# Kernel tuning notes

Hardware: AMD Instinct MI355X
Metric: run time of the kernel (lower is better)

## Reference

```python
import jax, jax.numpy as jnp
import numpy as np

HID = 128
H = 96
W = 96
WS = 6      # window_size
SS = 3      # shift_size
LN_EPS = 1e-5


def _layer_norm(x, g, b):
    m = x.mean(-1, keepdims=True)
    v = ((x - m) ** 2).mean(-1, keepdims=True)
    return (x - m) / jnp.sqrt(v + LN_EPS) * g + b


def _block(x, Wm, bm, g, bg):
    # Linear -> LayerNorm -> GELU (dropout is identity at inference)
    return jax.nn.gelu(_layer_norm(x @ Wm + bm, g, bg), approximate=False)


def _window_context(grid, Wt, bt, gt, bgt):
    # grid: [B, H, W, D]. Window partition + mean over the ws*ws tokens is
    # equivalent to a mean over each (ws, ws) tile; broadcasting back is a repeat.
    B, Hh, Ww, D = grid.shape
    nh, nw = Hh // WS, Ww // WS
    win_mean = grid.reshape(B, nh, WS, nw, WS, D).mean(axis=(2, 4))  # [B, nh, nw, D]
    tok = _block(win_mean, Wt, bt, gt, bgt)                          # token_proj
    return jnp.repeat(jnp.repeat(tok, WS, axis=1), WS, axis=2)       # [B, H, W, D]


def setup_inputs() -> dict:
    key = jax.random.key(0)
    ks = jax.random.split(key, 8)
    B = 32
    s = 1.0 / np.sqrt(HID)
    inp = {
        "h_pixel": jax.random.normal(ks[0], (B, H * W, HID), dtype=jnp.float32),
        "node_mask": jnp.ones((B, H * W), dtype=jnp.float32),
        # token_proj: Linear(D,D) + LayerNorm(D)
        "Wt": jax.random.normal(ks[1], (HID, HID), dtype=jnp.float32) * s,
        "bt": jnp.zeros((HID,), jnp.float32),
        "gt": jnp.ones((HID,), jnp.float32),
        "bgt": jnp.zeros((HID,), jnp.float32),
        # fuse: Linear(D,D) + LayerNorm(D)  (regular_shifted_sum -> fuse_in = D)
        "Wf": jax.random.normal(ks[2], (HID, HID), dtype=jnp.float32) * s,
        "bf": jnp.zeros((HID,), jnp.float32),
        "gf": jnp.ones((HID,), jnp.float32),
        "bgf": jnp.zeros((HID,), jnp.float32),
        # out_proj: Linear(D,D) + LayerNorm(D)
        "Wo": jax.random.normal(ks[3], (HID, HID), dtype=jnp.float32) * s,
        "bo": jnp.zeros((HID,), jnp.float32),
        "go": jnp.ones((HID,), jnp.float32),
        "bgo": jnp.zeros((HID,), jnp.float32),
    }
    return inp


def reference(h_pixel, node_mask, Wt, bt, gt, bgt, Wf, bf, gf, bgf, Wo, bo, go, bgo):
    B, N, D = h_pixel.shape
    grid = h_pixel.reshape(B, H, W, D)
    reg = _window_context(grid, Wt, bt, gt, bgt)
    shifted = jnp.roll(grid, (-SS, -SS), axis=(1, 2))
    sh = _window_context(shifted, Wt, bt, gt, bgt)
    sh = jnp.roll(sh, (SS, SS), axis=(1, 2))
    ctx = _block(reg + sh, Wf, bf, gf, bgf)     # fuse
    out = _block(ctx, Wo, bo, go, bgo)          # out_proj
    out = out.reshape(B, N, D) * node_mask[..., None]
    return out
```

## Files before the change

### kernel.cpp

```cpp
#include <hip/hip_runtime.h>
#include <hip/hip_bf16.h>


#define DEVFN static __device__ __forceinline__

typedef __attribute__((ext_vector_type(8))) short bf16x8;
typedef __attribute__((ext_vector_type(16))) float f32x16;

DEVFN float gelu_exact(float x) {
  return 0.5f * x * (1.0f + erff(x * 0.70710678118654752f));
}

DEVFN unsigned short f2bf(float f) {
  unsigned int u = __float_as_uint(f);
  u = (u + 0x7FFFu + ((u >> 16) & 1u)) >> 16;
  return (unsigned short)u;
}

DEVFN float bf2f(unsigned short u) {
  return __uint_as_float((unsigned int)u << 16);
}

DEVFN void add4(float4& a, const float4 v) {
  a.x += v.x; a.y += v.y; a.z += v.z; a.w += v.w;
}
DEVFN void fma4(float4& a, const float4 v, float m) {
  a.x = fmaf(v.x, m, a.x); a.y = fmaf(v.y, m, a.y);
  a.z = fmaf(v.z, m, a.z); a.w = fmaf(v.w, m, a.w);
}

__global__ __launch_bounds__(512) void k_tile3(const float* __restrict__ h,
                                               unsigned short* __restrict__ S3) {
  const int b  = blockIdx.x >> 5;
  const int ry = blockIdx.x & 31;
  const int w    = threadIdx.x >> 6;
  const int lane = threadIdx.x & 63;
  const int half = lane >> 5;
  const int ch4  = (lane & 31) << 2;
  const float mlo = half ? 0.f : 1.f;
  const float mhi = 1.f - mlo;

  float4 acc[4];
  #pragma unroll
  for (int t = 0; t < 4; ++t) acc[t] = make_float4(0.f, 0.f, 0.f, 0.f);

  #pragma unroll
  for (int yy = 0; yy < 3; ++yy) {
    const float* rp =
        h + ((size_t)(b * 9216 + (3 * ry + yy) * 96 + 12 * w + half) * 128 + ch4);
    #pragma unroll
    for (int j = 0; j < 6; ++j) {
      const float4 v = *reinterpret_cast<const float4*>(rp + j * 256);
      if (j == 0)      add4(acc[0], v);
      else if (j == 2) add4(acc[1], v);
      else if (j == 3) add4(acc[2], v);
      else if (j == 5) add4(acc[3], v);
      else if (j == 1) { fma4(acc[0], v, mlo); fma4(acc[1], v, mhi); }
      else             { fma4(acc[2], v, mlo); fma4(acc[3], v, mhi); }
    }
  }

  #pragma unroll
  for (int t = 0; t < 4; ++t) {
    float4 s = acc[t];
    s.x += __shfl_xor(s.x, 32, 64);
    s.y += __shfl_xor(s.y, 32, 64);
    s.z += __shfl_xor(s.z, 32, 64);
    s.w += __shfl_xor(s.w, 32, 64);
    if (half == 0) {
      short4 pk;
      pk.x = (short)f2bf(s.x); pk.y = (short)f2bf(s.y);
      pk.z = (short)f2bf(s.z); pk.w = (short)f2bf(s.w);
      *reinterpret_cast<short4*>(
          &S3[((size_t)(b * 32 + ry) * 32 + 4 * w + t) * 128 + ch4]) = pk;
    }
  }
}

DEVFN void stage_w_bf(unsigned short* __restrict__ wl,
                      const float* __restrict__ W, int tid) {
  #pragma unroll
  for (int p = 0; p < 4; ++p) {
    const int i = tid + p * 512;
    const int kp = i >> 5;
    const int n4 = (i & 31) * 4;
    const float4 r0 = *reinterpret_cast<const float4*>(W + (size_t)(2 * kp) * 128 + n4);
    const float4 r1 = *reinterpret_cast<const float4*>(W + (size_t)(2 * kp + 1) * 128 + n4);
    const float a0[4] = {r0.x, r0.y, r0.z, r0.w};
    const float a1[4] = {r1.x, r1.y, r1.z, r1.w};
    #pragma unroll
    for (int j = 0; j < 4; ++j) {
      const unsigned int pk =
          (unsigned int)f2bf(a0[j]) | ((unsigned int)f2bf(a1[j]) << 16);
      *reinterpret_cast<unsigned int*>(&wl[(n4 + j) * 136 + 2 * kp]) = pk;
    }
  }
}

DEVFN f32x16 mfma_tile(const unsigned short* __restrict__ xrow,
                       const unsigned short* __restrict__ wrow) {
  f32x16 acc;
  #pragma unroll
  for (int r = 0; r < 16; ++r) acc[r] = 0.f;
  #pragma unroll
  for (int kk = 0; kk < 8; ++kk) {
    const bf16x8 a = *reinterpret_cast<const bf16x8*>(xrow + kk * 16);
    const bf16x8 bb = *reinterpret_cast<const bf16x8*>(wrow + kk * 16);
    acc = __builtin_amdgcn_mfma_f32_32x32x16_bf16(a, bb, acc, 0, 0, 0);
  }
  return acc;
}

DEVFN void write_raw(float* __restrict__ raw, const f32x16 acc,
                     int tg, int cg, int lane) {
  const int n  = cg * 32 + (lane & 31);
  const int mb = tg * 32 + 4 * (lane >> 5);
  #pragma unroll
  for (int r = 0; r < 16; ++r) {
    const int mm = mb + (r & 3) + 8 * (r >> 2);
    raw[mm * 132 + n] = acc[r];
  }
}

__global__ __launch_bounds__(512) void k_tok(const unsigned short* __restrict__ S3,
    const float* __restrict__ Wt, const float* __restrict__ bt,
    const float* __restrict__ gt, const float* __restrict__ bgt,
    float* __restrict__ tok) {
  __shared__ __align__(16) unsigned short xs_bf[64 * 136];
  __shared__ __align__(16) unsigned short wl[128 * 136];
  float* raw = reinterpret_cast<float*>(wl);

  const int tid = threadIdx.x;
  const int t0 = blockIdx.x * 64;
  const int s  = t0 >> 13;
  const int b  = (t0 >> 8) & 31;
  const int wyx = t0 & 255;

  const unsigned short* Sb = S3 + (size_t)b * 131072;
  #pragma unroll
  for (int p = 0; p < 2; ++p) {
    const int i = tid + p * 512;
    const int tt = i >> 4, c8 = (i & 15) * 8;
    const int idx = wyx + tt;
    const int wy = idx >> 4, wx = idx & 15;
    int ry0, ry1, c0, c1;
    if (s == 0) { ry0 = 2 * wy;     ry1 = 2 * wy + 1;        c0 = 2 * wx;     c1 = 2 * wx + 1; }
    else        { ry0 = 2 * wy + 1; ry1 = (2 * wy + 2) & 31; c0 = 2 * wx + 1; c1 = (2 * wx + 2) & 31; }
    const bf16x8 v00 = *reinterpret_cast<const bf16x8*>(Sb + ((size_t)(ry0 * 32 + c0) * 128 + c8));
    const bf16x8 v01 = *reinterpret_cast<const bf16x8*>(Sb + ((size_t)(ry0 * 32 + c1) * 128 + c8));
    const bf16x8 v10 = *reinterpret_cast<const bf16x8*>(Sb + ((size_t)(ry1 * 32 + c0) * 128 + c8));
    const bf16x8 v11 = *reinterpret_cast<const bf16x8*>(Sb + ((size_t)(ry1 * 32 + c1) * 128 + c8));
    bf16x8 pk;
    #pragma unroll
    for (int j = 0; j < 8; ++j) {
      const float sum = bf2f((unsigned short)v00[j]) + bf2f((unsigned short)v01[j]) +
                        bf2f((unsigned short)v10[j]) + bf2f((unsigned short)v11[j]);
      pk[j] = (short)f2bf(sum * (1.f / 36.f));
    }
    *reinterpret_cast<bf16x8*>(&xs_bf[tt * 136 + c8]) = pk;
  }
  stage_w_bf(wl, Wt, tid);
  __syncthreads();

  const int lane = tid & 63;
  const int w = tid >> 6;
  const int tg = w >> 2, cg = w & 3;
  const unsigned short* xrow = &xs_bf[(tg * 32 + (lane & 31)) * 136 + 8 * (lane >> 5)];
  const unsigned short* wrow = &wl[(cg * 32 + (lane & 31)) * 136 + 8 * (lane >> 5)];

  const f32x16 acc = mfma_tile(xrow, wrow);
  __syncthreads();
  write_raw(raw, acc, tg, cg, lane);
  __syncthreads();

  {
    const int tt = tid >> 3, cb = tid & 7;
    float v[16];
    float s2 = 0.f, q = 0.f;
    #pragma unroll
    for (int i = 0; i < 4; ++i) {
      const int col = 4 * cb + 32 * i;
      const float4 rv = *reinterpret_cast<const float4*>(&raw[tt * 132 + col]);
      const float4 bv = *reinterpret_cast<const float4*>(bt + col);
      v[4 * i + 0] = rv.x + bv.x; v[4 * i + 1] = rv.y + bv.y;
      v[4 * i + 2] = rv.z + bv.z; v[4 * i + 3] = rv.w + bv.w;
    }
    #pragma unroll
    for (int e = 0; e < 16; ++e) { s2 += v[e]; q += v[e] * v[e]; }
    s2 += __shfl_xor(s2, 1, 8); q += __shfl_xor(q, 1, 8);
    s2 += __shfl_xor(s2, 2, 8); q += __shfl_xor(q, 2, 8);
    s2 += __shfl_xor(s2, 4, 8); q += __shfl_xor(q, 4, 8);
    const float mean = s2 * (1.f / 128.f);
    const float var  = q * (1.f / 128.f) - mean * mean;
    const float inv  = rsqrtf(var + 1e-5f);
    #pragma unroll
    for (int i = 0; i < 4; ++i) {
      const int col = 4 * cb + 32 * i;
      const float4 gv = *reinterpret_cast<const float4*>(gt + col);
      const float4 ev = *reinterpret_cast<const float4*>(bgt + col);
      float4 ov;
      ov.x = gelu_exact((v[4 * i + 0] - mean) * inv * gv.x + ev.x);
      ov.y = gelu_exact((v[4 * i + 1] - mean) * inv * gv.y + ev.y);
      ov.z = gelu_exact((v[4 * i + 2] - mean) * inv * gv.z + ev.z);
      ov.w = gelu_exact((v[4 * i + 3] - mean) * inv * gv.w + ev.w);
      *reinterpret_cast<float4*>(tok + (size_t)(t0 + tt) * 128 + col) = ov;
    }
  }
}

__global__ __launch_bounds__(512) void k_fuse_out(const float* __restrict__ tok,
    const float* __restrict__ Wf, const float* __restrict__ bfv,
    const float* __restrict__ gf, const float* __restrict__ bgf,
    const float* __restrict__ Wo, const float* __restrict__ bo,
    const float* __restrict__ go, const float* __restrict__ bgo,
    const float* __restrict__ mask, float* __restrict__ out) {
  __shared__ __align__(16) unsigned short xs_bf[64 * 136];
  __shared__ __align__(16) unsigned short wl[128 * 136];
  float* raw = reinterpret_cast<float*>(wl);

  const int tid = threadIdx.x;
  const int b = blockIdx.x >> 4;
  const int m = blockIdx.x & 15;
  const int lane = tid & 63;
  const int w = tid >> 6;
  const int tg = w >> 2, cg = w & 3;

  const float* tokR = tok + (size_t)b * 32768 + (size_t)m * 2048;
  const float* tokS = tok + 1048576 + (size_t)b * 32768;

  #pragma unroll
  for (int p = 0; p < 2; ++p) {
    const int i = tid + p * 512;
    const int t = i >> 4, c8 = (i & 15) * 8;
    const int gx = t & 31, gy = 2 * m + (t >> 5);
    const int wx  = gx >> 1;
    const int wxs = ((gx + 31) & 31) >> 1;
    const int wys = ((gy + 31) & 31) >> 1;
    const float* pr = tokR + (size_t)wx * 128 + c8;
    const float* ps = tokS + (size_t)(wys * 16 + wxs) * 128 + c8;
    bf16x8 pk;
    #pragma unroll
    for (int j = 0; j < 8; ++j)
      pk[j] = (short)f2bf(pr[j] + ps[j]);
    *reinterpret_cast<bf16x8*>(&xs_bf[t * 136 + c8]) = pk;
  }
  stage_w_bf(wl, Wf, tid);
  __syncthreads();

  const unsigned short* xrow = &xs_bf[(tg * 32 + (lane & 31)) * 136 + 8 * (lane >> 5)];
  const unsigned short* wrow = &wl[(cg * 32 + (lane & 31)) * 136 + 8 * (lane >> 5)];

  const f32x16 acc1 = mfma_tile(xrow, wrow);
  __syncthreads();
  write_raw(raw, acc1, tg, cg, lane);
  __syncthreads();

  {
    const int tt = tid >> 3, cb = tid & 7;
    float v[16];
    float s = 0.f, q = 0.f;
    #pragma unroll
    for (int i = 0; i < 4; ++i) {
      const int col = 4 * cb + 32 * i;
      const float4 rv = *reinterpret_cast<const float4*>(&raw[tt * 132 + col]);
      const float4 bv = *reinterpret_cast<const float4*>(bfv + col);
      v[4 * i + 0] = rv.x + bv.x; v[4 * i + 1] = rv.y + bv.y;
      v[4 * i + 2] = rv.z + bv.z; v[4 * i + 3] = rv.w + bv.w;
    }
    #pragma unroll
    for (int e = 0; e < 16; ++e) { s += v[e]; q += v[e] * v[e]; }
    s += __shfl_xor(s, 1, 8); q += __shfl_xor(q, 1, 8);
    s += __shfl_xor(s, 2, 8); q += __shfl_xor(q, 2, 8);
    s += __shfl_xor(s, 4, 8); q += __shfl_xor(q, 4, 8);
    const float mean = s * (1.f / 128.f);
    const float var  = q * (1.f / 128.f) - mean * mean;
    const float inv  = rsqrtf(var + 1e-5f);
    __syncthreads();
    #pragma unroll
    for (int i = 0; i < 4; ++i) {
      const int col = 4 * cb + 32 * i;
      const float4 gv = *reinterpret_cast<const float4*>(gf + col);
      const float4 ev = *reinterpret_cast<const float4*>(bgf + col);
      short4 pk;
      pk.x = (short)f2bf(gelu_exact((v[4 * i + 0] - mean) * inv * gv.x + ev.x));
      pk.y = (short)f2bf(gelu_exact((v[4 * i + 1] - mean) * inv * gv.y + ev.y));
      pk.z = (short)f2bf(gelu_exact((v[4 * i + 2] - mean) * inv * gv.z + ev.z));
      pk.w = (short)f2bf(gelu_exact((v[4 * i + 3] - mean) * inv * gv.w + ev.w));
      *reinterpret_cast<short4*>(&xs_bf[tt * 136 + col]) = pk;
    }
  }
  __syncthreads();
  stage_w_bf(wl, Wo, tid);
  __syncthreads();

  const f32x16 acc2 = mfma_tile(xrow, wrow);
  __syncthreads();
  write_raw(raw, acc2, tg, cg, lane);
  __syncthreads();

  {
    const int tt = tid >> 3, cb = tid & 7;
    float v[16];
    float s = 0.f, q = 0.f;
    #pragma unroll
    for (int i = 0; i < 4; ++i) {
      const int col = 4 * cb + 32 * i;
      const float4 rv = *reinterpret_cast<const float4*>(&raw[tt * 132 + col]);
      const float4 bv = *reinterpret_cast<const float4*>(bo + col);
      v[4 * i + 0] = rv.x + bv.x; v[4 * i + 1] = rv.y + bv.y;
      v[4 * i + 2] = rv.z + bv.z; v[4 * i + 3] = rv.w + bv.w;
    }
    #pragma unroll
    for (int e = 0; e < 16; ++e) { s += v[e]; q += v[e] * v[e]; }
    s += __shfl_xor(s, 1, 8); q += __shfl_xor(q, 1, 8);
    s += __shfl_xor(s, 2, 8); q += __shfl_xor(q, 2, 8);
    s += __shfl_xor(s, 4, 8); q += __shfl_xor(q, 4, 8);
    const float mean = s * (1.f / 128.f);
    const float var  = q * (1.f / 128.f) - mean * mean;
    const float inv  = rsqrtf(var + 1e-5f);
    #pragma unroll
    for (int i = 0; i < 4; ++i) {
      const int col = 4 * cb + 32 * i;
      const float4 gv = *reinterpret_cast<const float4*>(go + col);
      const float4 ev = *reinterpret_cast<const float4*>(bgo + col);
      v[4 * i + 0] = gelu_exact((v[4 * i + 0] - mean) * inv * gv.x + ev.x);
      v[4 * i + 1] = gelu_exact((v[4 * i + 1] - mean) * inv * gv.y + ev.y);
      v[4 * i + 2] = gelu_exact((v[4 * i + 2] - mean) * inv * gv.z + ev.z);
      v[4 * i + 3] = gelu_exact((v[4 * i + 3] - mean) * inv * gv.w + ev.w);
    }
    const int gx = tt & 31, gy = 2 * m + (tt >> 5);
    #pragma unroll
    for (int py = 0; py < 3; ++py) {
      const int y = 3 * gy + py;
      #pragma unroll
      for (int px = 0; px < 3; ++px) {
        const int x = 3 * gx + px;
        const size_t pix = (size_t)b * 9216 + (size_t)y * 96 + x;
        const float mv = mask[pix];
        #pragma unroll
        for (int i = 0; i < 4; ++i) {
          const int col = 4 * cb + 32 * i;
          *reinterpret_cast<float4*>(out + pix * 128 + col) =
              make_float4(v[4 * i + 0] * mv, v[4 * i + 1] * mv,
                          v[4 * i + 2] * mv, v[4 * i + 3] * mv);
        }
      }
    }
  }
}

extern "C" void kernel_launch(void* const* d_in, const int* in_sizes, int n_in,
                              void* d_out, int out_size, void* d_ws, size_t ws_size,
                              hipStream_t stream) {
  (void)in_sizes; (void)n_in; (void)out_size; (void)ws_size;
  const float* h    = (const float*)d_in[0];
  const float* mask = (const float*)d_in[1];
  const float* Wt   = (const float*)d_in[2];
  const float* bt   = (const float*)d_in[3];
  const float* gt   = (const float*)d_in[4];
  const float* bgt  = (const float*)d_in[5];
  const float* Wf   = (const float*)d_in[6];
  const float* bfv  = (const float*)d_in[7];
  const float* gf   = (const float*)d_in[8];
  const float* bgf  = (const float*)d_in[9];
  const float* Wo   = (const float*)d_in[10];
  const float* bo   = (const float*)d_in[11];
  const float* go   = (const float*)d_in[12];
  const float* bgo  = (const float*)d_in[13];

  unsigned short* S3 = (unsigned short*)d_ws;
  float* tok = (float*)((char*)d_ws + (size_t)8 * 1024 * 1024);
  float* out = (float*)d_out;

  hipLaunchKernelGGL(k_tile3, dim3(1024), dim3(512), 0, stream, h, S3);
  hipLaunchKernelGGL(k_tok, dim3(256), dim3(512), 0, stream,
                     S3, Wt, bt, gt, bgt, tok);
  hipLaunchKernelGGL(k_fuse_out, dim3(512), dim3(512), 0, stream,
                     tok, Wf, bfv, gf, bgf, Wo, bo, go, bgo, mask, out);
}
```

Baseline: 91.57 us.

## Shrink fuse_out blocks to 32 tokens and stage weights in K halves

Each k_fuse_out block now handles one grid row of 32 tokens with 256 threads instead of 64 tokens with 512, and the launch doubles to 1024 blocks. Each 128x128 weight is staged into shared memory in two 64-row K halves, with the MFMA accumulation split across them. The shared-memory footprint per block is roughly halved and a launch-bounds occupancy hint is added, so more blocks can be resident to hide latency from the heavy output stores. The cost is that every weight is converted and staged twice as often in total, plus extra barriers between the K halves.

```diff
diff --git a/kernel.cpp b/kernel.cpp
--- a/kernel.cpp
+++ b/kernel.cpp
@@ -97,6 +97,26 @@
   }
 }
 
+DEVFN void stage_w_half(unsigned short* __restrict__ wl,
+                        const float* __restrict__ W, int krow0, int tid) {
+  #pragma unroll
+  for (int p = 0; p < 4; ++p) {
+    const int i = tid + p * 256;
+    const int kp = i >> 5;
+    const int n4 = (i & 31) * 4;
+    const float4 r0 = *reinterpret_cast<const float4*>(W + (size_t)(krow0 + 2 * kp) * 128 + n4);
+    const float4 r1 = *reinterpret_cast<const float4*>(W + (size_t)(krow0 + 2 * kp + 1) * 128 + n4);
+    const float a0[4] = {r0.x, r0.y, r0.z, r0.w};
+    const float a1[4] = {r1.x, r1.y, r1.z, r1.w};
+    #pragma unroll
+    for (int j = 0; j < 4; ++j) {
+      const unsigned int pk =
+          (unsigned int)f2bf(a0[j]) | ((unsigned int)f2bf(a1[j]) << 16);
+      *reinterpret_cast<unsigned int*>(&wl[(n4 + j) * 68 + 2 * kp]) = pk;
+    }
+  }
+}
+
 DEVFN f32x16 mfma_tile(const unsigned short* __restrict__ xrow,
                        const unsigned short* __restrict__ wrow) {
   f32x16 acc;
@@ -109,6 +129,16 @@
     acc = __builtin_amdgcn_mfma_f32_32x32x16_bf16(a, bb, acc, 0, 0, 0);
   }
   return acc;
+}
+
+DEVFN void mfma_tile4(const unsigned short* __restrict__ xrow,
+                      const unsigned short* __restrict__ wrow, f32x16& acc) {
+  #pragma unroll
+  for (int kk = 0; kk < 4; ++kk) {
+    const bf16x8 a = *reinterpret_cast<const bf16x8*>(xrow + kk * 16);
+    const bf16x8 bb = *reinterpret_cast<const bf16x8*>(wrow + kk * 16);
+    acc = __builtin_amdgcn_mfma_f32_32x32x16_bf16(a, bb, acc, 0, 0, 0);
+  }
 }
 
 DEVFN void write_raw(float* __restrict__ raw, const f32x16 acc,
@@ -208,51 +238,58 @@
   }
 }
 
-__global__ __launch_bounds__(512) void k_fuse_out(const float* __restrict__ tok,
+__global__ __launch_bounds__(256, 6) void k_fuse_out(const float* __restrict__ tok,
     const float* __restrict__ Wf, const float* __restrict__ bfv,
     const float* __restrict__ gf, const float* __restrict__ bgf,
     const float* __restrict__ Wo, const float* __restrict__ bo,
     const float* __restrict__ go, const float* __restrict__ bgo,
     const float* __restrict__ mask, float* __restrict__ out) {
-  __shared__ __align__(16) unsigned short xs_bf[64 * 136];
-  __shared__ __align__(16) unsigned short wl[128 * 136];
+  __shared__ __align__(16) unsigned short xs_bf[32 * 136];
+  __shared__ __align__(16) unsigned short wl[128 * 68];
   float* raw = reinterpret_cast<float*>(wl);
 
   const int tid = threadIdx.x;
-  const int b = blockIdx.x >> 4;
-  const int m = blockIdx.x & 15;
+  const int b  = blockIdx.x >> 5;
+  const int gy = blockIdx.x & 31;
   const int lane = tid & 63;
-  const int w = tid >> 6;
-  const int tg = w >> 2, cg = w & 3;
-
-  const float* tokR = tok + (size_t)b * 32768 + (size_t)m * 2048;
-  const float* tokS = tok + 1048576 + (size_t)b * 32768;
+  const int cg = tid >> 6;
+
+  const int wy  = gy >> 1;
+  const int wys = ((gy + 31) & 31) >> 1;
+  const float* tokR = tok + (size_t)b * 32768 + (size_t)wy * 2048;
+  const float* tokS = tok + 1048576 + (size_t)b * 32768 + (size_t)wys * 2048;
 
   #pragma unroll
   for (int p = 0; p < 2; ++p) {
-    const int i = tid + p * 512;
+    const int i = tid + p * 256;
     const int t = i >> 4, c8 = (i & 15) * 8;
-    const int gx = t & 31, gy = 2 * m + (t >> 5);
-    const int wx  = gx >> 1;
-    const int wxs = ((gx + 31) & 31) >> 1;
-    const int wys = ((gy + 31) & 31) >> 1;
+    const int wx  = t >> 1;
+    const int wxs = ((t + 31) & 31) >> 1;
     const float* pr = tokR + (size_t)wx * 128 + c8;
-    const float* ps = tokS + (size_t)(wys * 16 + wxs) * 128 + c8;
+    const float* ps = tokS + (size_t)wxs * 128 + c8;
     bf16x8 pk;
     #pragma unroll
     for (int j = 0; j < 8; ++j)
       pk[j] = (short)f2bf(pr[j] + ps[j]);
     *reinterpret_cast<bf16x8*>(&xs_bf[t * 136 + c8]) = pk;
   }
-  stage_w_bf(wl, Wf, tid);
-  __syncthreads();
-
-  const unsigned short* xrow = &xs_bf[(tg * 32 + (lane & 31)) * 136 + 8 * (lane >> 5)];
-  const unsigned short* wrow = &wl[(cg * 32 + (lane & 31)) * 136 + 8 * (lane >> 5)];
-
-  const f32x16 acc1 = mfma_tile(xrow, wrow);
-  __syncthreads();
-  write_raw(raw, acc1, tg, cg, lane);
+  stage_w_half(wl, Wf, 0, tid);
+  __syncthreads();
+
+  const unsigned short* xrow = &xs_bf[(lane & 31) * 136 + 8 * (lane >> 5)];
+  const unsigned short* wrow = &wl[(cg * 32 + (lane & 31)) * 68 + 8 * (lane >> 5)];
+
+  f32x16 acc;
+  #pragma unroll
+  for (int r = 0; r < 16; ++r) acc[r] = 0.f;
+
+  mfma_tile4(xrow, wrow, acc);
+  __syncthreads();
+  stage_w_half(wl, Wf, 64, tid);
+  __syncthreads();
+  mfma_tile4(xrow + 64, wrow, acc);
+  __syncthreads();
+  write_raw(raw, acc, 0, cg, lane);
   __syncthreads();
 
   {
@@ -275,7 +312,6 @@
     const float mean = s * (1.f / 128.f);
     const float var  = q * (1.f / 128.f) - mean * mean;
     const float inv  = rsqrtf(var + 1e-5f);
-    __syncthreads();
     #pragma unroll
     for (int i = 0; i < 4; ++i) {
       const int col = 4 * cb + 32 * i;
@@ -290,12 +326,18 @@
     }
   }
   __syncthreads();
-  stage_w_bf(wl, Wo, tid);
-  __syncthreads();
-
-  const f32x16 acc2 = mfma_tile(xrow, wrow);
-  __syncthreads();
-  write_raw(raw, acc2, tg, cg, lane);
+
+  stage_w_half(wl, Wo, 0, tid);
+  __syncthreads();
+  #pragma unroll
+  for (int r = 0; r < 16; ++r) acc[r] = 0.f;
+  mfma_tile4(xrow, wrow, acc);
+  __syncthreads();
+  stage_w_half(wl, Wo, 64, tid);
+  __syncthreads();
+  mfma_tile4(xrow + 64, wrow, acc);
+  __syncthreads();
+  write_raw(raw, acc, 0, cg, lane);
   __syncthreads();
 
   {
@@ -328,7 +370,7 @@
       v[4 * i + 2] = gelu_exact((v[4 * i + 2] - mean) * inv * gv.z + ev.z);
       v[4 * i + 3] = gelu_exact((v[4 * i + 3] - mean) * inv * gv.w + ev.w);
     }
-    const int gx = tt & 31, gy = 2 * m + (tt >> 5);
+    const int gx = tt;
     #pragma unroll
     for (int py = 0; py < 3; ++py) {
       const int y = 3 * gy + py;
@@ -375,6 +417,6 @@
   hipLaunchKernelGGL(k_tile3, dim3(1024), dim3(512), 0, stream, h, S3);
   hipLaunchKernelGGL(k_tok, dim3(256), dim3(512), 0, stream,
                      S3, Wt, bt, gt, bgt, tok);
-  hipLaunchKernelGGL(k_fuse_out, dim3(512), dim3(512), 0, stream,
+  hipLaunchKernelGGL(k_fuse_out, dim3(1024), dim3(256), 0, stream,
                      tok, Wf, bfv, gf, bgf, Wo, bo, go, bgo, mask, out);
 }
```

Result: slower. 94.82 us (+3.6%).

## Pre-convert fuse/out weights to bf16 LDS images and split fused kernel in two

Applied to the files above, without the earlier changes.

Adds a tiny prep kernel that converts Wf and Wo once into padded bf16 images matching the LDS layout, so each block copies them with plain uint4 loads instead of converting per block. The fused fuse+out kernel is split into k_fuse, which writes a bf16 ctx tile to the workspace, and k_out, which reads it back. This removes the in-kernel weight conversion and one barrier sequence, but adds two launches and an extra global round trip for ctx. The old monolithic kernel is kept as a fallback when the workspace is too small.

```diff
diff --git a/kernel.cpp b/kernel.cpp
--- a/kernel.cpp
+++ b/kernel.cpp
@@ -27,6 +27,27 @@
 DEVFN void fma4(float4& a, const float4 v, float m) {
   a.x = fmaf(v.x, m, a.x); a.y = fmaf(v.y, m, a.y);
   a.z = fmaf(v.z, m, a.z); a.w = fmaf(v.w, m, a.w);
+}
+
+__global__ __launch_bounds__(512) void k_wprep(const float* __restrict__ Wf,
+    const float* __restrict__ Wo, unsigned int* __restrict__ imgs) {
+  const float* W = blockIdx.x ? Wo : Wf;
+  unsigned int* img = imgs + (size_t)blockIdx.x * 8704;
+  const int tid = threadIdx.x;
+  #pragma unroll
+  for (int p = 0; p < 4; ++p) {
+    const int i = tid + p * 512;
+    const int kp = i >> 5;
+    const int n4 = (i & 31) * 4;
+    const float4 r0 = *reinterpret_cast<const float4*>(W + (size_t)(2 * kp) * 128 + n4);
+    const float4 r1 = *reinterpret_cast<const float4*>(W + (size_t)(2 * kp + 1) * 128 + n4);
+    const float a0[4] = {r0.x, r0.y, r0.z, r0.w};
+    const float a1[4] = {r1.x, r1.y, r1.z, r1.w};
+    #pragma unroll
+    for (int j = 0; j < 4; ++j)
+      img[(n4 + j) * 68 + kp] =
+          (unsigned int)f2bf(a0[j]) | ((unsigned int)f2bf(a1[j]) << 16);
+  }
 }
 
 __global__ __launch_bounds__(512) void k_tile3(const float* __restrict__ h,
@@ -208,12 +229,10 @@
   }
 }
 
-__global__ __launch_bounds__(512) void k_fuse_out(const float* __restrict__ tok,
-    const float* __restrict__ Wf, const float* __restrict__ bfv,
-    const float* __restrict__ gf, const float* __restrict__ bgf,
-    const float* __restrict__ Wo, const float* __restrict__ bo,
-    const float* __restrict__ go, const float* __restrict__ bgo,
-    const float* __restrict__ mask, float* __restrict__ out) {
+__global__ __launch_bounds__(512) void k_fuse(const float* __restrict__ tok,
+    const unsigned int* __restrict__ wimg,
+    const float* __restrict__ bfv, const float* __restrict__ gf,
+    const float* __restrict__ bgf, unsigned short* __restrict__ ctx) {
   __shared__ __align__(16) unsigned short xs_bf[64 * 136];
   __shared__ __align__(16) unsigned short wl[128 * 136];
   float* raw = reinterpret_cast<float*>(wl);
@@ -244,17 +263,19 @@
       pk[j] = (short)f2bf(pr[j] + ps[j]);
     *reinterpret_cast<bf16x8*>(&xs_bf[t * 136 + c8]) = pk;
   }
-  stage_w_bf(wl, Wf, tid);
+  for (int i = tid; i < 2176; i += 512)
+    reinterpret_cast<uint4*>(wl)[i] = reinterpret_cast<const uint4*>(wimg)[i];
   __syncthreads();
 
   const unsigned short* xrow = &xs_bf[(tg * 32 + (lane & 31)) * 136 + 8 * (lane >> 5)];
   const unsigned short* wrow = &wl[(cg * 32 + (lane & 31)) * 136 + 8 * (lane >> 5)];
 
-  const f32x16 acc1 = mfma_tile(xrow, wrow);
-  __syncthreads();
-  write_raw(raw, acc1, tg, cg, lane);
-  __syncthreads();
-
+  const f32x16 acc = mfma_tile(xrow, wrow);
+  __syncthreads();
+  write_raw(raw, acc, tg, cg, lane);
+  __syncthreads();
+
+  unsigned short* cblk = ctx + (size_t)blockIdx.x * 8704;
   {
     const int tt = tid >> 3, cb = tid & 7;
     float v[16];
@@ -275,7 +296,6 @@
     const float mean = s * (1.f / 128.f);
     const float var  = q * (1.f / 128.f) - mean * mean;
     const float inv  = rsqrtf(var + 1e-5f);
-    __syncthreads();
     #pragma unroll
     for (int i = 0; i < 4; ++i) {
       const int col = 4 * cb + 32 * i;
@@ -286,16 +306,40 @@
       pk.y = (short)f2bf(gelu_exact((v[4 * i + 1] - mean) * inv * gv.y + ev.y));
       pk.z = (short)f2bf(gelu_exact((v[4 * i + 2] - mean) * inv * gv.z + ev.z));
       pk.w = (short)f2bf(gelu_exact((v[4 * i + 3] - mean) * inv * gv.w + ev.w));
-      *reinterpret_cast<short4*>(&xs_bf[tt * 136 + col]) = pk;
-    }
-  }
-  __syncthreads();
-  stage_w_bf(wl, Wo, tid);
-  __syncthreads();
-
-  const f32x16 acc2 = mfma_tile(xrow, wrow);
-  __syncthreads();
-  write_raw(raw, acc2, tg, cg, lane);
+      *reinterpret_cast<short4*>(&cblk[tt * 136 + col]) = pk;
+    }
+  }
+}
+
+__global__ __launch_bounds__(512) void k_out(const unsigned short* __restrict__ ctx,
+    const unsigned int* __restrict__ wimg,
+    const float* __restrict__ bo, const float* __restrict__ go,
+    const float* __restrict__ bgo,
+    const float* __restrict__ mask, float* __restrict__ out) {
+  __shared__ __align__(16) unsigned short xs_bf[64 * 136];
+  __shared__ __align__(16) unsigned short wl[128 * 136];
+  float* raw = reinterpret_cast<float*>(wl);
+
+  const int tid = threadIdx.x;
+  const int b = blockIdx.x >> 4;
+  const int m = blockIdx.x & 15;
+  const int lane = tid & 63;
+  const int w = tid >> 6;
+  const int tg = w >> 2, cg = w & 3;
+
+  const uint4* csrc = reinterpret_cast<const uint4*>(ctx + (size_t)blockIdx.x * 8704);
+  for (int i = tid; i < 1088; i += 512)
+    reinterpret_cast<uint4*>(xs_bf)[i] = csrc[i];
+  for (int i = tid; i < 2176; i += 512)
+    reinterpret_cast<uint4*>(wl)[i] = reinterpret_cast<const uint4*>(wimg)[i];
+  __syncthreads();
+
+  const unsigned short* xrow = &xs_bf[(tg * 32 + (lane & 31)) * 136 + 8 * (lane >> 5)];
+  const unsigned short* wrow = &wl[(cg * 32 + (lane & 31)) * 136 + 8 * (lane >> 5)];
+
+  const f32x16 acc = mfma_tile(xrow, wrow);
+  __syncthreads();
+  write_raw(raw, acc, tg, cg, lane);
   __syncthreads();
 
   {
@@ -349,10 +393,151 @@
   }
 }
 
+__global__ __launch_bounds__(512) void k_fuse_out_mono(const float* __restrict__ tok,
+    const float* __restrict__ Wf, const float* __restrict__ bfv,
+    const float* __restrict__ gf, const float* __restrict__ bgf,
+    const float* __restrict__ Wo, const float* __restrict__ bo,
+    const float* __restrict__ go, const float* __restrict__ bgo,
+    const float* __restrict__ mask, float* __restrict__ out) {
+  __shared__ __align__(16) unsigned short xs_bf[64 * 136];
+  __shared__ __align__(16) unsigned short wl[128 * 136];
+  float* raw = reinterpret_cast<float*>(wl);
+
+  const int tid = threadIdx.x;
+  const int b = blockIdx.x >> 4;
+  const int m = blockIdx.x & 15;
+  const int lane = tid & 63;
+  const int w = tid >> 6;
+  const int tg = w >> 2, cg = w & 3;
+
+  const float* tokR = tok + (size_t)b * 32768 + (size_t)m * 2048;
+  const float* tokS = tok + 1048576 + (size_t)b * 32768;
+
+  #pragma unroll
+  for (int p = 0; p < 2; ++p) {
+    const int i = tid + p * 512;
+    const int t = i >> 4, c8 = (i & 15) * 8;
+    const int gx = t & 31, gy = 2 * m + (t >> 5);
+    const int wx  = gx >> 1;
+    const int wxs = ((gx + 31) & 31) >> 1;
+    const int wys = ((gy + 31) & 31) >> 1;
+    const float* pr = tokR + (size_t)wx * 128 + c8;
+    const float* ps = tokS + (size_t)(wys * 16 + wxs) * 128 + c8;
+    bf16x8 pk;
+    #pragma unroll
+    for (int j = 0; j < 8; ++j)
+      pk[j] = (short)f2bf(pr[j] + ps[j]);
+    *reinterpret_cast<bf16x8*>(&xs_bf[t * 136 + c8]) = pk;
+  }
+  stage_w_bf(wl, Wf, tid);
+  __syncthreads();
+
+  const unsigned short* xrow = &xs_bf[(tg * 32 + (lane & 31)) * 136 + 8 * (lane >> 5)];
+  const unsigned short* wrow = &wl[(cg * 32 + (lane & 31)) * 136 + 8 * (lane >> 5)];
+
+  const f32x16 acc1 = mfma_tile(xrow, wrow);
+  __syncthreads();
+  write_raw(raw, acc1, tg, cg, lane);
+  __syncthreads();
+
+  {
+    const int tt = tid >> 3, cb = tid & 7;
+    float v[16];
+    float s = 0.f, q = 0.f;
+    #pragma unroll
+    for (int i = 0; i < 4; ++i) {
+      const int col = 4 * cb + 32 * i;
+      const float4 rv = *reinterpret_cast<const float4*>(&raw[tt * 132 + col]);
+      const float4 bv = *reinterpret_cast<const float4*>(bfv + col);
+      v[4 * i + 0] = rv.x + bv.x; v[4 * i + 1] = rv.y + bv.y;
+      v[4 * i + 2] = rv.z + bv.z; v[4 * i + 3] = rv.w + bv.w;
+    }
+    #pragma unroll
+    for (int e = 0; e < 16; ++e) { s += v[e]; q += v[e] * v[e]; }
+    s += __shfl_xor(s, 1, 8); q += __shfl_xor(q, 1, 8);
+    s += __shfl_xor(s, 2, 8); q += __shfl_xor(q, 2, 8);
+    s += __shfl_xor(s, 4, 8); q += __shfl_xor(q, 4, 8);
+    const float mean = s * (1.f / 128.f);
+    const float var  = q * (1.f / 128.f) - mean * mean;
+    const float inv  = rsqrtf(var + 1e-5f);
+    __syncthreads();
+    #pragma unroll
+    for (int i = 0; i < 4; ++i) {
+      const int col = 4 * cb + 32 * i;
+      const float4 gv = *reinterpret_cast<const float4*>(gf + col);
+      const float4 ev = *reinterpret_cast<const float4*>(bgf + col);
+      short4 pk;
+      pk.x = (short)f2bf(gelu_exact((v[4 * i + 0] - mean) * inv * gv.x + ev.x));
+      pk.y = (short)f2bf(gelu_exact((v[4 * i + 1] - mean) * inv * gv.y + ev.y));
+      pk.z = (short)f2bf(gelu_exact((v[4 * i + 2] - mean) * inv * gv.z + ev.z));
+      pk.w = (short)f2bf(gelu_exact((v[4 * i + 3] - mean) * inv * gv.w + ev.w));
+      *reinterpret_cast<short4*>(&xs_bf[tt * 136 + col]) = pk;
+    }
+  }
+  __syncthreads();
+  stage_w_bf(wl, Wo, tid);
+  __syncthreads();
+
+  const f32x16 acc2 = mfma_tile(xrow, wrow);
+  __syncthreads();
+  write_raw(raw, acc2, tg, cg, lane);
+  __syncthreads();
+
+  {
+    const int tt = tid >> 3, cb = tid & 7;
+    float v[16];
+    float s = 0.f, q = 0.f;
+    #pragma unroll
+    for (int i = 0; i < 4; ++i) {
+      const int col = 4 * cb + 32 * i;
+      const float4 rv = *reinterpret_cast<const float4*>(&raw[tt * 132 + col]);
+      const float4 bv = *reinterpret_cast<const float4*>(bo + col);
+      v[4 * i + 0] = rv.x + bv.x; v[4 * i + 1] = rv.y + bv.y;
+      v[4 * i + 2] = rv.z + bv.z; v[4 * i + 3] = rv.w + bv.w;
+    }
+    #pragma unroll
+    for (int e = 0; e < 16; ++e) { s += v[e]; q += v[e] * v[e]; }
+    s += __shfl_xor(s, 1, 8); q += __shfl_xor(q, 1, 8);
+    s += __shfl_xor(s, 2, 8); q += __shfl_xor(q, 2, 8);
+    s += __shfl_xor(s, 4, 8); q += __shfl_xor(q, 4, 8);
+    const float mean = s * (1.f / 128.f);
+    const float var  = q * (1.f / 128.f) - mean * mean;
+    const float inv  = rsqrtf(var + 1e-5f);
+    #pragma unroll
+    for (int i = 0; i < 4; ++i) {
+      const int col = 4 * cb + 32 * i;
+      const float4 gv = *reinterpret_cast<const float4*>(go + col);
+      const float4 ev = *reinterpret_cast<const float4*>(bgo + col);
+      v[4 * i + 0] = gelu_exact((v[4 * i + 0] - mean) * inv * gv.x + ev.x);
+      v[4 * i + 1] = gelu_exact((v[4 * i + 1] - mean) * inv * gv.y + ev.y);
+      v[4 * i + 2] = gelu_exact((v[4 * i + 2] - mean) * inv * gv.z + ev.z);
+      v[4 * i + 3] = gelu_exact((v[4 * i + 3] - mean) * inv * gv.w + ev.w);
+    }
+    const int gx = tt & 31, gy = 2 * m + (tt >> 5);
+    #pragma unroll
+    for (int py = 0; py < 3; ++py) {
+      const int y = 3 * gy + py;
+      #pragma unroll
+      for (int px = 0; px < 3; ++px) {
+        const int x = 3 * gx + px;
+        const size_t pix = (size_t)b * 9216 + (size_t)y * 96 + x;
+        const float mv = mask[pix];
+        #pragma unroll
+        for (int i = 0; i < 4; ++i) {
+          const int col = 4 * cb + 32 * i;
+          *reinterpret_cast<float4*>(out + pix * 128 + col) =
+              make_float4(v[4 * i + 0] * mv, v[4 * i + 1] * mv,
+                          v[4 * i + 2] * mv, v[4 * i + 3] * mv);
+        }
+      }
+    }
+  }
+}
+
 extern "C" void kernel_launch(void* const* d_in, const int* in_sizes, int n_in,
                               void* d_out, int out_size, void* d_ws, size_t ws_size,
                               hipStream_t stream) {
-  (void)in_sizes; (void)n_in; (void)out_size; (void)ws_size;
+  (void)in_sizes; (void)n_in; (void)out_size;
   const float* h    = (const float*)d_in[0];
   const float* mask = (const float*)d_in[1];
   const float* Wt   = (const float*)d_in[2];
@@ -372,9 +557,23 @@
   float* tok = (float*)((char*)d_ws + (size_t)8 * 1024 * 1024);
   float* out = (float*)d_out;
 
+  const size_t NEED = (size_t)16 * 1024 * 1024 + 131072 + (size_t)512 * 17408;
+
   hipLaunchKernelGGL(k_tile3, dim3(1024), dim3(512), 0, stream, h, S3);
   hipLaunchKernelGGL(k_tok, dim3(256), dim3(512), 0, stream,
                      S3, Wt, bt, gt, bgt, tok);
-  hipLaunchKernelGGL(k_fuse_out, dim3(512), dim3(512), 0, stream,
-                     tok, Wf, bfv, gf, bgf, Wo, bo, go, bgo, mask, out);
-}
+
+  if (ws_size >= NEED) {
+    unsigned int* imgs = (unsigned int*)((char*)d_ws + (size_t)16 * 1024 * 1024);
+    unsigned short* ctx =
+        (unsigned short*)((char*)d_ws + (size_t)16 * 1024 * 1024 + 131072);
+    hipLaunchKernelGGL(k_wprep, dim3(2), dim3(512), 0, stream, Wf, Wo, imgs);
+    hipLaunchKernelGGL(k_fuse, dim3(512), dim3(512), 0, stream,
+                       tok, imgs, bfv, gf, bgf, ctx);
+    hipLaunchKernelGGL(k_out, dim3(512), dim3(512), 0, stream,
+                       ctx, imgs + 8704, bo, go, bgo, mask, out);
+  } else {
+    hipLaunchKernelGGL(k_fuse_out_mono, dim3(512), dim3(512), 0, stream,
+                       tok, Wf, bfv, gf, bgf, Wo, bo, go, bgo, mask, out);
+  }
+}
```

Result: slower. 103.0 us (+12.5%).
